# Kernel tuning notes

Hardware: AMD Instinct MI355X
Metric: run time of the kernel (lower is better)

The kernel has to match this reference:

```python
import jax, jax.numpy as jnp
import numpy as np

PS = 10            # patchsize
ADJ = PS // 2      # use_adj offset (patches centered on query pixel)
K = 7              # neighbors
WS = 29            # search window
R = WS // 2
SCALE = 1.0        # dist_scale


def setup_inputs() -> dict:
    key = jax.random.key(0)
    k1, k2, k3 = jax.random.split(key, 3)
    x = jax.random.normal(k1, (1, 16, 96, 96), jnp.float32)
    xe = jax.random.normal(k2, (1, 8, 96, 96), jnp.float32)
    ye = jax.random.normal(k3, (1, 8, 96, 96), jnp.float32)
    return {"x": x, "xe": xe, "ye": ye}


def _patch_pad(img):
    # zero border for patch reads (dnls iUnfold border='zero', adj=ps//2)
    return jnp.pad(img, ((0, 0), (ADJ, PS - 1 - ADJ), (ADJ, PS - 1 - ADJ)))


def _boxsum(a, h, w):
    # sum over ps x ps windows via integral image; a: (h+PS-1, w+PS-1) -> (h, w)
    c = jnp.pad(jnp.cumsum(jnp.cumsum(a, 0), 1), ((1, 0), (1, 0)))
    return c[PS:PS + h, PS:PS + w] - c[:h, PS:PS + w] - c[PS:PS + h, :w] + c[:h, :w]


def _extract_patches(imgp, h, w):
    # imgp: (C, h+PS-1, w+PS-1) patch-padded -> (h*w, C*PS*PS)
    rows = jnp.arange(h)[:, None] + jnp.arange(PS)[None, :]
    cols = jnp.arange(w)[:, None] + jnp.arange(PS)[None, :]
    pat = imgp[:, rows][:, :, :, cols]          # (C, h, PS, w, PS)
    return pat.transpose(1, 3, 0, 2, 4).reshape(h * w, -1)


def _forward(x, xe, ye):
    x, xe, ye = x[0], xe[0], ye[0]              # t = 1
    pad1 = lambda a: jnp.pad(a, ((0, 0), (1, 1), (1, 1)))  # F.pad(.., (1,1,1,1))
    x, xe, ye = pad1(x), pad1(xe), pad1(ye)
    y = x                                        # y=None -> y=x path
    c, h, w = x.shape
    H2, W2 = h + PS - 1, w + PS - 1

    # ---- L2 patch search over WS x WS displacement window ----
    yep = _patch_pad(ye)
    xep = _patch_pad(xe)
    xebig = jnp.pad(xep, ((0, 0), (R, R), (R, R)))
    disp = jnp.arange(WS * WS)
    dys = disp // WS - R
    dxs = disp % WS - R

    def dist_for(dy, dx):
        xs = jax.lax.dynamic_slice(xebig, (0, R + dy, R + dx), (xep.shape[0], H2, W2))
        sq = jnp.sum((yep - xs) ** 2, axis=0)   # (H2, W2)
        return _boxsum(sq, h, w)                # (h, w)

    dists = jax.vmap(dist_for)(dys, dxs)        # (WS*WS, h, w)

    # invalidate out-of-bounds centers + self (remove_self=True)
    ni = jnp.arange(h)[None, :, None] + dys[:, None, None]
    nj = jnp.arange(w)[None, None, :] + dxs[:, None, None]
    valid = (ni >= 0) & (ni < h) & (nj >= 0) & (nj < w) & \
            ((dys != 0) | (dxs != 0))[:, None, None]
    dists = jnp.where(valid, dists, jnp.float32(1e10))

    dq = dists.reshape(WS * WS, h * w).T        # (Q, WS*WS)
    neg, idx = jax.lax.top_k(-dq, K)            # k smallest dists; neg = -l2
    Wgt = jax.nn.softmax(SCALE * neg, axis=-1)  # softmax(scale * (-dists))

    # absolute flat neighbor indices
    qi = jnp.arange(h * w) // w
    qj = jnp.arange(h * w) % w
    flat = (qi[:, None] + dys[idx]) * w + (qj[:, None] + dxs[idx])  # (Q, K)

    # ---- indexed weighted aggregation of x patches ----
    xp = _extract_patches(_patch_pad(x), h, w)  # (Q, c*PS*PS)
    z_patches = jnp.einsum('qk,qkc->qc', Wgt, xp[flat])

    # ---- fold with overlap count (iFoldz: vid / zvid) ----
    zp = z_patches.reshape(h, w, c, PS, PS).transpose(2, 0, 1, 3, 4)
    vid = jnp.zeros((c, H2, W2), x.dtype)
    for oy in range(PS):
        for ox in range(PS):
            vid = vid.at[:, oy:oy + h, ox:ox + w].add(zp[:, :, :, oy, ox])
    ra, ca = jnp.arange(H2), jnp.arange(W2)
    cnt_r = (jnp.minimum(ra, h - 1) - jnp.maximum(ra - PS + 1, 0) + 1).astype(x.dtype)
    cnt_c = (jnp.minimum(ca, w - 1) - jnp.maximum(ca - PS + 1, 0) + 1).astype(x.dtype)
    zvid = cnt_r[:, None] * cnt_c[None, :]
    z = vid[:, ADJ:ADJ + h, ADJ:ADJ + w] / zvid[ADJ:ADJ + h, ADJ:ADJ + w][None]

    z = z - y
    out = jnp.concatenate([y, z], axis=0)       # (2c, h, w)
    return out[None, :, 1:-1, 1:-1]             # crop the border pad


def reference(x, xe, ye):
    return _forward(x, xe, ye)
```

## Files before the change

### kernel.cpp

```cpp
#include <hip/hip_runtime.h>

#define PS   10
#define KNN  7
#define WSZ  29
#define RR   14
#define IH   96
#define IW   96
#define CH   16
#define CE   8
#define HH   98
#define QN   (HH*HH)
#define ND   (WSZ*WSZ)
#define XTW  124
#define XTP  14
#define YEW  107
#define YEH  112
#define XEW  144
#define XEH  140
#define QP   9800

#define OFF_SV   8241856ull
#define OFF_SD   (OFF_SV + 76832ull)
#define OFF_CV   (OFF_SD + 76832ull)
#define OFF_CI   (OFF_CV + 307328ull)
#define OFF_XT   (OFF_CI + 307328ull)
#define OFF_YEP  (OFF_XT + 246016ull)
#define OFF_XEP  (OFF_YEP + 95872ull)

__device__ __forceinline__ int imin(int a, int b){ return a<b?a:b; }
__device__ __forceinline__ int imax(int a, int b){ return a>b?a:b; }

__global__ __launch_bounds__(256) void k_prep(const float* __restrict__ x,
                                              const float* __restrict__ xe,
                                              const float* __restrict__ ye,
                                              float* __restrict__ xT,
                                              float* __restrict__ xeP,
                                              float* __restrict__ yeP) {
    int t = blockIdx.x*256 + threadIdx.x;
    if (t < XTW*XTW) {
        int u = t / XTW, v = t % XTW;
        int ui = u - XTP, vi = v - XTP;
        bool inb = ((unsigned)ui < (unsigned)IH) && ((unsigned)vi < (unsigned)IW);
        int off = inb ? (ui*IW + vi) : 0;
        float4* dst = (float4*)(xT + (size_t)t*CH);
        #pragma unroll
        for (int c4 = 0; c4 < 4; ++c4) {
            float4 val;
            val.x = inb ? x[(c4*4+0)*IH*IW + off] : 0.f;
            val.y = inb ? x[(c4*4+1)*IH*IW + off] : 0.f;
            val.z = inb ? x[(c4*4+2)*IH*IW + off] : 0.f;
            val.w = inb ? x[(c4*4+3)*IH*IW + off] : 0.f;
            dst[c4] = val;
        }
        return;
    }
    t -= XTW*XTW;
    if (t < YEH*YEW) {
        int i = t / YEW, j = t % YEW;
        bool inb = ((unsigned)(i-6) < (unsigned)IH) && ((unsigned)(j-6) < (unsigned)IW);
        int off = inb ? ((i-6)*IW + (j-6)) : 0;
        float4* dst = (float4*)(yeP + (size_t)t*CE);
        #pragma unroll
        for (int c4 = 0; c4 < 2; ++c4) {
            float4 val;
            val.x = inb ? ye[(c4*4+0)*IH*IW + off] : 0.f;
            val.y = inb ? ye[(c4*4+1)*IH*IW + off] : 0.f;
            val.z = inb ? ye[(c4*4+2)*IH*IW + off] : 0.f;
            val.w = inb ? ye[(c4*4+3)*IH*IW + off] : 0.f;
            dst[c4] = val;
        }
        return;
    }
    t -= YEH*YEW;
    if (t < XEH*XEW) {
        int i = t / XEW, j = t % XEW;
        bool inb = ((unsigned)(i-20) < (unsigned)IH) && ((unsigned)(j-20) < (unsigned)IW);
        int off = inb ? ((i-20)*IW + (j-20)) : 0;
        float4* dst = (float4*)(xeP + (size_t)t*CE);
        #pragma unroll
        for (int c4 = 0; c4 < 2; ++c4) {
            float4 val;
            val.x = inb ? xe[(c4*4+0)*IH*IW + off] : 0.f;
            val.y = inb ? xe[(c4*4+1)*IH*IW + off] : 0.f;
            val.z = inb ? xe[(c4*4+2)*IH*IW + off] : 0.f;
            val.w = inb ? xe[(c4*4+3)*IH*IW + off] : 0.f;
            dst[c4] = val;
        }
    }
}

__global__ __launch_bounds__(128, 4) void k_dist(const float* __restrict__ xeP,
                                                 const float* __restrict__ yeP,
                                                 float* __restrict__ dist) {
    __shared__ float cs[2][4][72];

    int b     = blockIdx.x;
    int dx_i  = b % 29;
    int rem   = b / 29;
    int strip = rem % 7;
    int dyg   = rem / 7;
    int y0s   = strip * 14;
    int tid   = threadIdx.x;
    int wid   = tid >> 6;
    int lane  = tid & 63;
    int col   = wid ? (43 + lane) : lane;
    int widx  = lane + (wid ? 3 : 0);

    int nun   = wid ? 12 : 13;
    int dyi_c = imin(lane / nun, 3);
    int u     = lane - dyi_c * nun;
    bool cact = lane < nun * 4;
    int x0u   = wid ? (52 + 4*u) : (4*u);
    bool full4 = (wid == 0) || (u < 11);
    const float* rdp = &cs[wid][dyi_c][ wid ? (12 + 4*u) : (4*u) ];
    int plane = dyg*4 + dyi_c;
    bool plane_ok = cact && (plane <= 28);
    int dy_c  = plane - 14;
    int dx    = dx_i - 14;
    bool selfd = (dy_c == 0) && (dx == 0);
    bool okx0 = (unsigned)(x0u+0+dx) < 98u;
    bool okx1 = (unsigned)(x0u+1+dx) < 98u;
    bool okx2 = (unsigned)(x0u+2+dx) < 98u;
    bool okx3 = (unsigned)(x0u+3+dx) < 98u;
    float* dout = dist + (size_t)(imin(plane,28)*29 + dx_i)*QP + x0u;

    const size_t xstep = (size_t)XEW*CE, ystep = (size_t)YEW*CE;
    const float* xload = xeP + ((size_t)(y0s + dyg*4)*XEW + (col + dx_i))*CE;
    const float* yload = yeP + ((size_t)y0s*YEW + col)*CE;

    float4 xr[5][2];
    #pragma unroll
    for (int r = 0; r < 4; ++r) {
        xr[r][0] = ((const float4*)xload)[0];
        xr[r][1] = ((const float4*)xload)[1];
        xload += xstep;
    }
    float wsum[4] = {0.f,0.f,0.f,0.f};
    float hist[4][10];

#define DSTEP(S) { \
    float4 xna = ((const float4*)xload)[0]; \
    float4 xnb = ((const float4*)xload)[1]; \
    xload += xstep; \
    float4 ya  = ((const float4*)yload)[0]; \
    float4 yb  = ((const float4*)yload)[1]; \
    yload += ystep; \
    xr[(S+4)%5][0] = xna; xr[(S+4)%5][1] = xnb; \
    _Pragma("unroll") \
    for (int dyi = 0; dyi < 4; ++dyi) { \
        float4 xa = xr[(S+dyi)%5][0]; \
        float4 xb = xr[(S+dyi)%5][1]; \
        float d0=ya.x-xa.x, d1=ya.y-xa.y, d2=ya.z-xa.z, d3=ya.w-xa.w; \
        float d4=yb.x-xb.x, d5=yb.y-xb.y, d6=yb.z-xb.z, d7=yb.w-xb.w; \
        float a = d0*d0; \
        a=fmaf(d1,d1,a); a=fmaf(d2,d2,a); a=fmaf(d3,d3,a); \
        a=fmaf(d4,d4,a); a=fmaf(d5,d5,a); a=fmaf(d6,d6,a); \
        a=fmaf(d7,d7,a); \
        float w = wsum[dyi] + a; \
        if ((S) >= 10) w -= hist[dyi][(S)%10]; \
        wsum[dyi] = w; \
        hist[dyi][(S)%10] = a; \
        cs[wid][dyi][widx] = w; \
    } \
    if ((S) >= 9 && plane_ok) { \
        float v0=rdp[0], v1=rdp[1], v2=rdp[2], v3=rdp[3]; \
        float v4=rdp[4], v5=rdp[5], v6=rdp[6], v7=rdp[7]; \
        float v8=rdp[8], v9=rdp[9], v10=rdp[10], v11=rdp[11], v12=rdp[12]; \
        float s0 = ((v0+v1)+(v2+v3)) + ((v4+v5)+(v6+v7)) + (v8+v9); \
        float s1 = s0 - v0 + v10; \
        float s2 = s1 - v1 + v11; \
        float s3 = s2 - v2 + v12; \
        int y0 = y0s + (S) - 9; \
        bool okr = ((unsigned)(y0 + dy_c) < 98u) && !selfd; \
        float4 o; \
        o.x = (okr && okx0) ? s0 : 1e10f; \
        o.y = (okr && okx1) ? s1 : 1e10f; \
        o.z = (okr && okx2) ? s2 : 1e10f; \
        o.w = (okr && okx3) ? s3 : 1e10f; \
        if (full4) *(float4*)(dout + y0*100) = o; \
        else       *(float2*)(dout + y0*100) = make_float2(o.x, o.y); \
    } \
}

    DSTEP(0)  DSTEP(1)  DSTEP(2)  DSTEP(3)  DSTEP(4)
    DSTEP(5)  DSTEP(6)  DSTEP(7)  DSTEP(8)  DSTEP(9)
    DSTEP(10) DSTEP(11) DSTEP(12) DSTEP(13) DSTEP(14)
    DSTEP(15) DSTEP(16) DSTEP(17) DSTEP(18) DSTEP(19)
    DSTEP(20) DSTEP(21) DSTEP(22)
#undef DSTEP
}

__global__ __launch_bounds__(256) void k_topkA(const float* __restrict__ dist,
                                               float* __restrict__ cv, int* __restrict__ ci) {
    __shared__ float lv[3*64*8];
    __shared__ int   lix[3*64*8];
    int wv = threadIdx.x >> 6, ln = threadIdx.x & 63;
    int qb = blockIdx.x % 151;
    int rg = blockIdx.x / 151;
    int q  = qb*64 + ln;
    int qq = q < QN ? q : QN-1;
    int y0 = qq / 98, x0 = qq - y0*98;
    int off = y0*100 + x0;

    int rbase = rg*210 + (rg > 0 ? 1 : 0);
    int ndr   = (rg == 0) ? 211 : 210;
    int s0 = rbase + wv*53;
    int s1 = imin(rbase + ndr, s0 + 53);

    float ld[KNN]; int li[KNN];
    #pragma unroll
    for (int k = 0; k < KNN; ++k) { ld[k] = 1e30f; li[k] = -1; }

    auto INS = [&](float v, int dsp) {
        float cvv = v; int cii = dsp;
        #pragma unroll
        for (int k = 0; k < KNN; ++k) {
            bool sw = cvv < ld[k];
            float tf = ld[k]; int ti = li[k];
            ld[k] = sw ? cvv : tf;  li[k] = sw ? cii : ti;
            cvv   = sw ? tf : cvv;  cii   = sw ? ti : cii;
        }
    };

    #pragma unroll 2
    for (int dd = s0; dd < s1; ++dd)
        INS(dist[(size_t)dd*QP + off], dd);

    if (wv) {
        int bse = ((wv-1)*64 + ln)*8;
        #pragma unroll
        for (int r = 0; r < KNN; ++r) { lv[bse+r] = ld[r]; lix[bse+r] = li[r]; }
    }
    __syncthreads();
    if (wv == 0 && q < QN) {
        #pragma unroll
        for (int w = 0; w < 3; ++w) {
            int bse = (w*64 + ln)*8;
            #pragma unroll
            for (int r = 0; r < KNN; ++r) INS(lv[bse+r], lix[bse+r]);
        }
        #pragma unroll
        for (int r = 0; r < KNN; ++r) {
            cv[(q*4 + rg)*8 + r] = ld[r];
            ci[(q*4 + rg)*8 + r] = li[r];
        }
    }
}

__global__ __launch_bounds__(256) void k_topkB(const float* __restrict__ cv,
                                               const int* __restrict__ ci,
                                               float* __restrict__ sv, int* __restrict__ sd) {
    int q = blockIdx.x*256 + threadIdx.x;
    if (q >= QN) return;

    float ld[KNN]; int li[KNN];
    #pragma unroll
    for (int k = 0; k < KNN; ++k) { ld[k] = 1e30f; li[k] = -1; }

    auto INS = [&](float v, int dsp) {
        float cvv = v; int cii = dsp;
        #pragma unroll
        for (int k = 0; k < KNN; ++k) {
            bool sw = cvv < ld[k];
            float tf = ld[k]; int ti = li[k];
            ld[k] = sw ? cvv : tf;  li[k] = sw ? cii : ti;
            cvv   = sw ? tf : cvv;  cii   = sw ? ti : cii;
        }
    };

    #pragma unroll
    for (int rg = 0; rg < 4; ++rg) {
        #pragma unroll
        for (int r = 0; r < KNN; ++r)
            INS(cv[(q*4 + rg)*8 + r], ci[(q*4 + rg)*8 + r]);
    }

    float e[KNN]; float ssum = 0.f;
    #pragma unroll
    for (int r = 0; r < KNN; ++r) { e[r] = __expf(ld[0] - ld[r]); ssum += e[r]; }
    float inv = 1.f / ssum;
    #pragma unroll
    for (int r = 0; r < KNN; ++r) {
        sv[q*8 + r] = e[r] * inv;
        int dsp = li[r];
        int dyk = dsp / WSZ - RR, dxk = dsp % WSZ - RR;
        sd[q*8 + r] = (dyk*XTW + dxk) * CH;
    }
}

__global__ __launch_bounds__(512) void k_agg(const float* __restrict__ xT,
                                             const float* __restrict__ wgt,
                                             const int* __restrict__ dlt,
                                             float* __restrict__ out) {
    __shared__ float2 lw[13*13*7];
    __shared__ float4 red[7*64];
    int tid = threadIdx.x;
    int tb = blockIdx.x;
    int ai0 = (tb / 24) * 4, bi0 = (tb % 24) * 4;

    for (int u = tid; u < 13*13*7; u += 512) {
        int lq = u / 7, k = u - lq*7;
        int lqi = lq / 13, lqj = lq - lqi*13;
        int qi = ai0 - 3 + lqi, qj = bi0 - 3 + lqj;
        bool ok = ((unsigned)qi < 98u) && ((unsigned)qj < 98u);
        int q = ok ? (qi*98 + qj) : 0;
        float w = ok ? wgt[q*8 + k] : 0.f;
        int  dl = ok ? dlt[q*8 + k] : 0;
        lw[u] = make_float2(w, __int_as_float(dl));
    }
    __syncthreads();

    int og   = tid >> 6;
    int rem  = tid & 63;
    int quad = rem & 3;
    int pl   = rem >> 2;
    int py   = pl >> 2, px = pl & 3;
    int ai = ai0 + py, bi = bi0 + px;
    int base = ((ai + XTP)*XTW + (bi + XTP))*CH + quad*4;

    float ax=0.f, ay=0.f, az=0.f, aw=0.f;
    #pragma unroll
    for (int c = 0; c < 13; ++c) {
        int u = og*13 + c;
        if (u >= 100) break;
        int oy = u / 10, ox = u - oy*10;
        int lq = (py + 9 - oy)*13 + (px + 9 - ox);
        const float2* f2p = lw + lq*7;
        #pragma unroll
        for (int k = 0; k < KNN; ++k) {
            float2 wd = f2p[k];
            int dl = __float_as_int(wd.y);
            const float4 xv = *(const float4*)(xT + base + dl);
            ax = fmaf(wd.x, xv.x, ax); ay = fmaf(wd.x, xv.y, ay);
            az = fmaf(wd.x, xv.z, az); aw = fmaf(wd.x, xv.w, aw);
        }
    }

    if (og) {
        float4 pr; pr.x=ax; pr.y=ay; pr.z=az; pr.w=aw;
        red[(og-1)*64 + rem] = pr;
    }
    __syncthreads();
    if (og == 0) {
        #pragma unroll
        for (int w = 0; w < 7; ++w) {
            float4 pr = red[w*64 + rem];
            ax += pr.x; ay += pr.y; az += pr.z; aw += pr.w;
        }
        int i = ai + 6, j = bi + 6;
        float cr = (float)(imin(i, 97) - imax(i - 9, 0) + 1);
        float cc = (float)(imin(j, 97) - imax(j - 9, 0) + 1);
        float inv = 1.f / (cr * cc);
        float4 xs = *(const float4*)(xT + base);
        int p = ai*IW + bi;
        int ch0 = quad*4;
        out[(ch0+0)*IH*IW + p] = xs.x;
        out[(ch0+1)*IH*IW + p] = xs.y;
        out[(ch0+2)*IH*IW + p] = xs.z;
        out[(ch0+3)*IH*IW + p] = xs.w;
        out[(16+ch0+0)*IH*IW + p] = ax*inv - xs.x;
        out[(16+ch0+1)*IH*IW + p] = ay*inv - xs.y;
        out[(16+ch0+2)*IH*IW + p] = az*inv - xs.z;
        out[(16+ch0+3)*IH*IW + p] = aw*inv - xs.w;
    }
}

extern "C" void kernel_launch(void* const* d_in, const int* in_sizes, int n_in,
                              void* d_out, int out_size, void* d_ws, size_t ws_size,
                              hipStream_t stream) {
    const float* x  = (const float*)d_in[0];
    const float* xe = (const float*)d_in[1];
    const float* ye = (const float*)d_in[2];
    float* out = (float*)d_out;
    float* ws  = (float*)d_ws;

    float* dist = ws;
    float* sv   = ws + OFF_SV;
    int*   sd   = (int*)(ws + OFF_SD);
    float* cv   = ws + OFF_CV;
    int*   ci   = (int*)(ws + OFF_CI);
    float* xT   = ws + OFF_XT;
    float* yeP  = ws + OFF_YEP;
    float* xeP  = ws + OFF_XEP;

    {
        int total = XTW*XTW + YEH*YEW + XEH*XEW;
        hipLaunchKernelGGL(k_prep, dim3((total + 255)/256), dim3(256), 0, stream,
                           x, xe, ye, xT, xeP, yeP);
    }
    hipLaunchKernelGGL(k_dist,  dim3(8*29*7), dim3(128), 0, stream, xeP, yeP, dist);
    hipLaunchKernelGGL(k_topkA, dim3(151*4), dim3(256), 0, stream, dist, cv, ci);
    hipLaunchKernelGGL(k_topkB, dim3((QN + 255)/256), dim3(256), 0, stream, cv, ci, sv, sd);
    hipLaunchKernelGGL(k_agg,   dim3(24*24), dim3(512), 0, stream, xT, sv, sd, out);
}
```

Baseline: 78.96 us.

## Fuse top-k merge and softmax into aggregation, store x gather table as bf16

Removes the separate k_topkB launch. Each aggregation block now merges the four partial top-k lists and computes the softmax weights for its 13x13 neighbourhood of queries directly into shared memory. The transposed x table used for patch gathers is stored in bf16, which halves gather bandwidth. The block shrinks to 256 threads, each accumulating 8 channels, and the exact x identity term is read from the original input. Trade-offs: merged top-k work is recomputed redundantly across overlapping block halos, and bf16 rounding adds error to the aggregated output.

```diff
diff --git a/kernel.cpp b/kernel.cpp
--- a/kernel.cpp
+++ b/kernel.cpp
@@ -19,21 +19,23 @@
 #define XEH  140
 #define QP   9800
 
-#define OFF_SV   8241856ull
-#define OFF_SD   (OFF_SV + 76832ull)
-#define OFF_CV   (OFF_SD + 76832ull)
+#define OFF_CV   8241856ull
 #define OFF_CI   (OFF_CV + 307328ull)
 #define OFF_XT   (OFF_CI + 307328ull)
-#define OFF_YEP  (OFF_XT + 246016ull)
+#define OFF_YEP  (OFF_XT + 123072ull)
 #define OFF_XEP  (OFF_YEP + 95872ull)
 
 __device__ __forceinline__ int imin(int a, int b){ return a<b?a:b; }
 __device__ __forceinline__ int imax(int a, int b){ return a>b?a:b; }
+__device__ __forceinline__ unsigned short f2bf(float f){
+    unsigned u = __float_as_uint(f);
+    return (unsigned short)((u + 0x7fffu + ((u >> 16) & 1u)) >> 16);
+}
 
 __global__ __launch_bounds__(256) void k_prep(const float* __restrict__ x,
                                               const float* __restrict__ xe,
                                               const float* __restrict__ ye,
-                                              float* __restrict__ xT,
+                                              unsigned short* __restrict__ xTb,
                                               float* __restrict__ xeP,
                                               float* __restrict__ yeP) {
     int t = blockIdx.x*256 + threadIdx.x;
@@ -42,16 +44,16 @@
         int ui = u - XTP, vi = v - XTP;
         bool inb = ((unsigned)ui < (unsigned)IH) && ((unsigned)vi < (unsigned)IW);
         int off = inb ? (ui*IW + vi) : 0;
-        float4* dst = (float4*)(xT + (size_t)t*CH);
-        #pragma unroll
-        for (int c4 = 0; c4 < 4; ++c4) {
-            float4 val;
-            val.x = inb ? x[(c4*4+0)*IH*IW + off] : 0.f;
-            val.y = inb ? x[(c4*4+1)*IH*IW + off] : 0.f;
-            val.z = inb ? x[(c4*4+2)*IH*IW + off] : 0.f;
-            val.w = inb ? x[(c4*4+3)*IH*IW + off] : 0.f;
-            dst[c4] = val;
-        }
+        unsigned d[8];
+        #pragma unroll
+        for (int j = 0; j < 8; ++j) {
+            float a = inb ? x[(2*j+0)*IH*IW + off] : 0.f;
+            float b = inb ? x[(2*j+1)*IH*IW + off] : 0.f;
+            d[j] = (unsigned)f2bf(a) | ((unsigned)f2bf(b) << 16);
+        }
+        uint4* dst = (uint4*)(xTb + (size_t)t*CH);
+        dst[0] = make_uint4(d[0], d[1], d[2], d[3]);
+        dst[1] = make_uint4(d[4], d[5], d[6], d[7]);
         return;
     }
     t -= XTW*XTW;
@@ -222,7 +224,7 @@
         }
     };
 
-    #pragma unroll 2
+    #pragma unroll 4
     for (int dd = s0; dd < s1; ++dd)
         INS(dist[(size_t)dd*QP + off], dd);
 
@@ -247,78 +249,69 @@
     }
 }
 
-__global__ __launch_bounds__(256) void k_topkB(const float* __restrict__ cv,
-                                               const int* __restrict__ ci,
-                                               float* __restrict__ sv, int* __restrict__ sd) {
-    int q = blockIdx.x*256 + threadIdx.x;
-    if (q >= QN) return;
-
-    float ld[KNN]; int li[KNN];
-    #pragma unroll
-    for (int k = 0; k < KNN; ++k) { ld[k] = 1e30f; li[k] = -1; }
-
-    auto INS = [&](float v, int dsp) {
-        float cvv = v; int cii = dsp;
-        #pragma unroll
-        for (int k = 0; k < KNN; ++k) {
-            bool sw = cvv < ld[k];
-            float tf = ld[k]; int ti = li[k];
-            ld[k] = sw ? cvv : tf;  li[k] = sw ? cii : ti;
-            cvv   = sw ? tf : cvv;  cii   = sw ? ti : cii;
-        }
-    };
-
-    #pragma unroll
-    for (int rg = 0; rg < 4; ++rg) {
-        #pragma unroll
-        for (int r = 0; r < KNN; ++r)
-            INS(cv[(q*4 + rg)*8 + r], ci[(q*4 + rg)*8 + r]);
-    }
-
-    float e[KNN]; float ssum = 0.f;
-    #pragma unroll
-    for (int r = 0; r < KNN; ++r) { e[r] = __expf(ld[0] - ld[r]); ssum += e[r]; }
-    float inv = 1.f / ssum;
-    #pragma unroll
-    for (int r = 0; r < KNN; ++r) {
-        sv[q*8 + r] = e[r] * inv;
-        int dsp = li[r];
-        int dyk = dsp / WSZ - RR, dxk = dsp % WSZ - RR;
-        sd[q*8 + r] = (dyk*XTW + dxk) * CH;
-    }
-}
-
-__global__ __launch_bounds__(512) void k_agg(const float* __restrict__ xT,
-                                             const float* __restrict__ wgt,
-                                             const int* __restrict__ dlt,
+__global__ __launch_bounds__(256) void k_agg(const float* __restrict__ x,
+                                             const unsigned short* __restrict__ xTb,
+                                             const float* __restrict__ cv,
+                                             const int* __restrict__ ci,
                                              float* __restrict__ out) {
-    __shared__ float2 lw[13*13*7];
-    __shared__ float4 red[7*64];
+    __shared__ float2 lw[169*7];
+    __shared__ float  red[7][8][32];
     int tid = threadIdx.x;
-    int tb = blockIdx.x;
+    int tb  = blockIdx.x;
     int ai0 = (tb / 24) * 4, bi0 = (tb % 24) * 4;
 
-    for (int u = tid; u < 13*13*7; u += 512) {
-        int lq = u / 7, k = u - lq*7;
-        int lqi = lq / 13, lqj = lq - lqi*13;
+    if (tid < 169) {
+        int lqi = tid / 13, lqj = tid - lqi*13;
         int qi = ai0 - 3 + lqi, qj = bi0 - 3 + lqj;
         bool ok = ((unsigned)qi < 98u) && ((unsigned)qj < 98u);
-        int q = ok ? (qi*98 + qj) : 0;
-        float w = ok ? wgt[q*8 + k] : 0.f;
-        int  dl = ok ? dlt[q*8 + k] : 0;
-        lw[u] = make_float2(w, __int_as_float(dl));
+        float ld[KNN]; int li[KNN];
+        #pragma unroll
+        for (int k = 0; k < KNN; ++k) { ld[k] = 1e30f; li[k] = -1; }
+        if (ok) {
+            int q = qi*98 + qj;
+            #pragma unroll
+            for (int rg = 0; rg < 4; ++rg) {
+                #pragma unroll
+                for (int r = 0; r < KNN; ++r) {
+                    float v  = cv[(q*4 + rg)*8 + r];
+                    int dsp  = ci[(q*4 + rg)*8 + r];
+                    float cvv = v; int cii = dsp;
+                    #pragma unroll
+                    for (int k = 0; k < KNN; ++k) {
+                        bool sw = cvv < ld[k];
+                        float tf = ld[k]; int ti = li[k];
+                        ld[k] = sw ? cvv : tf;  li[k] = sw ? cii : ti;
+                        cvv   = sw ? tf : cvv;  cii   = sw ? ti : cii;
+                    }
+                }
+            }
+            float e[KNN]; float ssum = 0.f;
+            #pragma unroll
+            for (int r = 0; r < KNN; ++r) { e[r] = __expf(ld[0] - ld[r]); ssum += e[r]; }
+            float inv = 1.f / ssum;
+            #pragma unroll
+            for (int r = 0; r < KNN; ++r) {
+                int dsp = li[r];
+                int dyk = dsp / WSZ - RR, dxk = dsp % WSZ - RR;
+                lw[tid*7 + r] = make_float2(e[r]*inv,
+                                            __int_as_float((dyk*XTW + dxk)*CH));
+            }
+        } else {
+            #pragma unroll
+            for (int r = 0; r < KNN; ++r) lw[tid*7 + r] = make_float2(0.f, 0.f);
+        }
     }
     __syncthreads();
 
-    int og   = tid >> 6;
-    int rem  = tid & 63;
-    int quad = rem & 3;
-    int pl   = rem >> 2;
+    int og   = tid >> 5;
+    int rem  = tid & 31;
+    int half = rem & 1;
+    int pl   = rem >> 1;
     int py   = pl >> 2, px = pl & 3;
     int ai = ai0 + py, bi = bi0 + px;
-    int base = ((ai + XTP)*XTW + (bi + XTP))*CH + quad*4;
-
-    float ax=0.f, ay=0.f, az=0.f, aw=0.f;
+    int baseu = ((ai + XTP)*XTW + (bi + XTP))*CH + half*8;
+
+    float acc[8] = {0.f,0.f,0.f,0.f,0.f,0.f,0.f,0.f};
     #pragma unroll
     for (int c = 0; c < 13; ++c) {
         int u = og*13 + c;
@@ -329,39 +322,43 @@
         #pragma unroll
         for (int k = 0; k < KNN; ++k) {
             float2 wd = f2p[k];
+            float w = wd.x;
             int dl = __float_as_int(wd.y);
-            const float4 xv = *(const float4*)(xT + base + dl);
-            ax = fmaf(wd.x, xv.x, ax); ay = fmaf(wd.x, xv.y, ay);
-            az = fmaf(wd.x, xv.z, az); aw = fmaf(wd.x, xv.w, aw);
+            const uint4 g = *(const uint4*)(xTb + baseu + dl);
+            acc[0] = fmaf(w, __uint_as_float(g.x << 16),          acc[0]);
+            acc[1] = fmaf(w, __uint_as_float(g.x & 0xffff0000u),  acc[1]);
+            acc[2] = fmaf(w, __uint_as_float(g.y << 16),          acc[2]);
+            acc[3] = fmaf(w, __uint_as_float(g.y & 0xffff0000u),  acc[3]);
+            acc[4] = fmaf(w, __uint_as_float(g.z << 16),          acc[4]);
+            acc[5] = fmaf(w, __uint_as_float(g.z & 0xffff0000u),  acc[5]);
+            acc[6] = fmaf(w, __uint_as_float(g.w << 16),          acc[6]);
+            acc[7] = fmaf(w, __uint_as_float(g.w & 0xffff0000u),  acc[7]);
         }
     }
 
     if (og) {
-        float4 pr; pr.x=ax; pr.y=ay; pr.z=az; pr.w=aw;
-        red[(og-1)*64 + rem] = pr;
+        #pragma unroll
+        for (int c = 0; c < 8; ++c) red[og-1][c][rem] = acc[c];
     }
     __syncthreads();
     if (og == 0) {
         #pragma unroll
-        for (int w = 0; w < 7; ++w) {
-            float4 pr = red[w*64 + rem];
-            ax += pr.x; ay += pr.y; az += pr.z; aw += pr.w;
-        }
+        for (int w = 0; w < 7; ++w)
+            #pragma unroll
+            for (int c = 0; c < 8; ++c) acc[c] += red[w][c][rem];
+
         int i = ai + 6, j = bi + 6;
         float cr = (float)(imin(i, 97) - imax(i - 9, 0) + 1);
         float cc = (float)(imin(j, 97) - imax(j - 9, 0) + 1);
         float inv = 1.f / (cr * cc);
-        float4 xs = *(const float4*)(xT + base);
         int p = ai*IW + bi;
-        int ch0 = quad*4;
-        out[(ch0+0)*IH*IW + p] = xs.x;
-        out[(ch0+1)*IH*IW + p] = xs.y;
-        out[(ch0+2)*IH*IW + p] = xs.z;
-        out[(ch0+3)*IH*IW + p] = xs.w;
-        out[(16+ch0+0)*IH*IW + p] = ax*inv - xs.x;
-        out[(16+ch0+1)*IH*IW + p] = ay*inv - xs.y;
-        out[(16+ch0+2)*IH*IW + p] = az*inv - xs.z;
-        out[(16+ch0+3)*IH*IW + p] = aw*inv - xs.w;
+        #pragma unroll
+        for (int c = 0; c < 8; ++c) {
+            int ch = half*8 + c;
+            float xv = x[ch*IH*IW + p];
+            out[ch*IH*IW + p] = xv;
+            out[(16 + ch)*IH*IW + p] = acc[c]*inv - xv;
+        }
     }
 }
 
@@ -375,21 +372,18 @@
     float* ws  = (float*)d_ws;
 
     float* dist = ws;
-    float* sv   = ws + OFF_SV;
-    int*   sd   = (int*)(ws + OFF_SD);
     float* cv   = ws + OFF_CV;
     int*   ci   = (int*)(ws + OFF_CI);
-    float* xT   = ws + OFF_XT;
+    unsigned short* xTb = (unsigned short*)(ws + OFF_XT);
     float* yeP  = ws + OFF_YEP;
     float* xeP  = ws + OFF_XEP;
 
     {
         int total = XTW*XTW + YEH*YEW + XEH*XEW;
         hipLaunchKernelGGL(k_prep, dim3((total + 255)/256), dim3(256), 0, stream,
-                           x, xe, ye, xT, xeP, yeP);
+                           x, xe, ye, xTb, xeP, yeP);
     }
     hipLaunchKernelGGL(k_dist,  dim3(8*29*7), dim3(128), 0, stream, xeP, yeP, dist);
     hipLaunchKernelGGL(k_topkA, dim3(151*4), dim3(256), 0, stream, dist, cv, ci);
-    hipLaunchKernelGGL(k_topkB, dim3((QN + 255)/256), dim3(256), 0, stream, cv, ci, sv, sd);
-    hipLaunchKernelGGL(k_agg,   dim3(24*24), dim3(512), 0, stream, xT, sv, sd, out);
-}
+    hipLaunchKernelGGL(k_agg,   dim3(24*24), dim3(256), 0, stream, x, xTb, cv, ci, out);
+}
```

Result: faster. 72.62 us (-8.0%).
